# Kernel optimization log

Measured on AMD Instinct MI355X. Metric: run time of the kernel, lower is better.

The kernel has to match this reference:

```python
import jax, jax.numpy as jnp
import numpy as np
import math

B, S, D_MODEL = 8, 1024, 1024
N_INPUT, N_PROCESS = 256, 512
N_HEADS, N_HEADS_IN = 8, 4
HIDDEN = 2 * N_INPUT  # combination_analyzer hidden dim (default n_input*2)
TEMP = 2.0            # router temperature buffer


def _mha(x, w_in, b_in, w_out, b_out, n_heads):
    """torch nn.MultiheadAttention (batch_first, eval mode) self-attention."""
    Bq, Sq, E = x.shape
    qkv = x @ w_in.T + b_in                      # [B,S,3E]
    q, k, v = jnp.split(qkv, 3, axis=-1)
    dh = E // n_heads
    sh = lambda t: t.reshape(Bq, Sq, n_heads, dh).transpose(0, 2, 1, 3)
    q, k, v = sh(q), sh(k), sh(v)
    scores = jnp.einsum('bhqd,bhkd->bhqk', q, k) * (1.0 / math.sqrt(dh))
    attn = jax.nn.softmax(scores, axis=-1)
    out = jnp.einsum('bhqk,bhkd->bhqd', attn, v).transpose(0, 2, 1, 3).reshape(Bq, Sq, E)
    return out @ w_out.T + b_out


def _ln(x, g, b, eps=1e-5):
    m = x.mean(-1, keepdims=True)
    v = ((x - m) ** 2).mean(-1, keepdims=True)
    return (x - m) / jnp.sqrt(v + eps) * g + b


def setup_inputs() -> dict:
    key = jax.random.key(0)
    ks = jax.random.split(key, 24)
    rn = lambda i, shape, s=0.02: jax.random.normal(ks[i], shape, jnp.float32) * s
    return {
        'x': jax.random.normal(ks[0], (B, S, D_MODEL), jnp.float32),
        # DynamicRouter attention (embed=d_model, heads=8)
        'r_in_w': rn(1, (3 * D_MODEL, D_MODEL)), 'r_in_b': jnp.zeros((3 * D_MODEL,), jnp.float32),
        'r_out_w': rn(2, (D_MODEL, D_MODEL)), 'r_out_b': jnp.zeros((D_MODEL,), jnp.float32),
        'aff_w': rn(3, (N_INPUT, D_MODEL)), 'aff_b': jnp.zeros((N_INPUT,), jnp.float32),
        # InputNeurons
        'patterns': rn(4, (N_INPUT, D_MODEL), 0.05),
        'i_in_w': rn(5, (3 * N_INPUT, N_INPUT)), 'i_in_b': jnp.zeros((3 * N_INPUT,), jnp.float32),
        'i_out_w': rn(6, (N_INPUT, N_INPUT)), 'i_out_b': jnp.zeros((N_INPUT,), jnp.float32),
        'ln_g': jnp.ones((N_INPUT,), jnp.float32), 'ln_b': jnp.zeros((N_INPUT,), jnp.float32),
        # ProcessNeurons
        'comb_w': rn(7, (N_PROCESS, N_INPUT), 0.05),
        'out_proj_w': rn(8, (N_PROCESS, D_MODEL), 0.05),
        'a1_w': rn(9, (HIDDEN, N_INPUT)), 'a1_b': jnp.zeros((HIDDEN,), jnp.float32),
        'a2_w': rn(10, (N_PROCESS, HIDDEN)), 'a2_b': jnp.zeros((N_PROCESS,), jnp.float32),
        'k_input': 128, 'k_process': 256,
    }


def reference(x, r_in_w, r_in_b, r_out_w, r_out_b, aff_w, aff_b, patterns,
              i_in_w, i_in_b, i_out_w, i_out_b, ln_g, ln_b,
              comb_w, out_proj_w, a1_w, a1_b, a2_w, a2_b, k_input, k_process):
    Bq = x.shape[0]
    # ---- DynamicRouter (eval mode: no gumbel noise, no score noise) ----
    context = _mha(x, r_in_w, r_in_b, r_out_w, r_out_b, N_HEADS)      # [B,S,D]
    affinity = context @ aff_w.T + aff_b                              # [B,S,N_INPUT]
    scores = affinity.max(axis=1)                                     # [B,N_INPUT]
    logits = scores / TEMP
    soft_w = jax.nn.softmax(logits, axis=-1)
    _, indices = jax.lax.top_k(logits, k_input)                       # [B,k_in]
    mask = jnp.zeros_like(soft_w).at[jnp.arange(Bq)[:, None], indices].set(1.0)
    masked = soft_w * mask
    weights = masked / (masked.sum(-1, keepdims=True) + 1e-8)         # [B,N_INPUT]
    # ---- InputNeurons (eval: dropout off) ----
    acts = jax.nn.gelu(context @ patterns.T, approximate=False)       # [B,S,N_INPUT]
    attn_out = _mha(acts, i_in_w, i_in_b, i_out_w, i_out_b, N_HEADS_IN)
    acts = _ln(acts + attn_out, ln_g, ln_b)
    # ---- Gather routed input neurons, weighted by routing weights ----
    sel_acts = jnp.take_along_axis(acts, indices[:, None, :], axis=2)  # [B,S,k_in]
    sel_w = jnp.take_along_axis(weights, indices, axis=1)              # [B,k_in]
    sel_acts = sel_acts * sel_w[:, None, :]
    # ---- ProcessNeurons ----
    # selected_weights[b,p,j] = comb_w[p, indices[b,j]]
    sel_cw = jnp.take(comb_w, indices, axis=1).transpose(1, 0, 2)      # [B,P,k_in]
    proc_acts = jax.nn.gelu(jnp.einsum('bsk,bpk->bsp', sel_acts, sel_cw), approximate=False)
    input_sel = jnp.zeros((Bq, N_INPUT), jnp.float32).at[jnp.arange(Bq)[:, None], indices].set(1.0)
    relevance = jax.nn.gelu(input_sel @ a1_w.T + a1_b, approximate=False) @ a2_w.T + a2_b  # [B,P]
    act_scores = proc_acts.max(axis=1)                                 # [B,P]
    final_scores = act_scores * jax.nn.sigmoid(relevance)
    _, pidx = jax.lax.top_k(final_scores, k_process)                   # [B,k_p]
    sel_proc = jnp.take_along_axis(proc_acts, pidx[:, None, :], axis=2)  # [B,S,k_p]
    sel_proj = out_proj_w[pidx]                                        # [B,k_p,D]
    out = jnp.einsum('bsk,bkd->bsd', sel_proc, sel_proj)               # [B,S,D]
    # ---- residual (eval: dropout identity) ----
    return x + out
```

## Files before the change

### kernel.cpp

```cpp
#include <hip/hip_runtime.h>
#include <hip/hip_bf16.h>
#include <math.h>

constexpr int NB = 8, NS = 1024, ND = 1024, NIN = 256, NPROC = 512, KIN = 128, KPROC = 256;

typedef __attribute__((ext_vector_type(8))) short bf16x8;
typedef __attribute__((ext_vector_type(4))) float f32x4;

#define VMCNT(n) asm volatile("s_waitcnt vmcnt(" #n ")" ::: "memory")
#define LGKMCNT(n) asm volatile("s_waitcnt lgkmcnt(" #n ")" ::: "memory")

__device__ inline float gelu_f(float x) {
    return 0.5f * x * (1.0f + erff(x * 0.7071067811865476f));
}
__device__ inline unsigned short f2b(float f) {
    __hip_bfloat16 h = __float2bfloat16(f);
    return *reinterpret_cast<unsigned short*>(&h);
}
__device__ inline void gload16(const void* g, void* l) {
    __builtin_amdgcn_global_load_lds(
        (const __attribute__((address_space(1))) void*)g,
        (__attribute__((address_space(3))) void*)l, 16, 0, 0);
}

__global__ __launch_bounds__(256)
void cvt_all_kernel(const float* __restrict__ x, const float* __restrict__ rin,
                    const float* __restrict__ rout, const float* __restrict__ affw,
                    const float* __restrict__ patt, const float* __restrict__ iin,
                    const float* __restrict__ iout, const float* __restrict__ aff_b,
                    unsigned short* __restrict__ xb, unsigned short* __restrict__ rinb,
                    unsigned short* __restrict__ routb, unsigned short* __restrict__ affbw,
                    unsigned short* __restrict__ pattb, unsigned short* __restrict__ iinb,
                    unsigned short* __restrict__ ioutb, float* __restrict__ biascat)
{
    if (blockIdx.x == 0) {
        int t = threadIdx.x;
        biascat[t] = aff_b[t];
        biascat[256 + t] = 0.f;
    }
    long gi = (long)blockIdx.x * 256 + threadIdx.x;
    long stride = (long)gridDim.x * 256;
    for (; gi < 3342336; gi += stride) {
        const float4* s; ushort4* d; long off;
        if (gi < 2097152)      { s = (const float4*)x;    d = (ushort4*)xb;    off = gi; }
        else if (gi < 2883584) { s = (const float4*)rin;  d = (ushort4*)rinb;  off = gi - 2097152; }
        else if (gi < 3145728) { s = (const float4*)rout; d = (ushort4*)routb; off = gi - 2883584; }
        else if (gi < 3211264) { s = (const float4*)affw; d = (ushort4*)affbw; off = gi - 3145728; }
        else if (gi < 3276800) { s = (const float4*)patt; d = (ushort4*)pattb; off = gi - 3211264; }
        else if (gi < 3325952) { s = (const float4*)iin;  d = (ushort4*)iinb;  off = gi - 3276800; }
        else                   { s = (const float4*)iout; d = (ushort4*)ioutb; off = gi - 3325952; }
        float4 v = s[off];
        ushort4 o;
        o.x = f2b(v.x); o.y = f2b(v.y); o.z = f2b(v.z); o.w = f2b(v.w);
        d[off] = o;
    }
}

__global__ __launch_bounds__(256)
void gemm128s(const unsigned short* __restrict__ A, int lda,
              const unsigned short* __restrict__ B, int ldb,
              const float* __restrict__ bias,
              unsigned short* __restrict__ C16, int ldc,
              int K, int nbx)
{
    __shared__ __align__(16) unsigned short Ab[3][128 * 32];
    __shared__ __align__(16) unsigned short Bb[3][128 * 32];
    int o = blockIdx.x;
    int cpx = gridDim.x >> 3;
    int swz = (o & 7) * cpx + (o >> 3);
    int by = swz / nbx, bx = swz - by * nbx;
    int row0 = by * 128, col0 = bx * 128;

    int t = threadIdx.x;
    int w = t >> 6, l = t & 63, l15 = l & 15, g = l >> 4;
    int wr = w >> 1, wc = w & 1;
    int NT = K >> 5;

    f32x4 acc[4][4];
#pragma unroll
    for (int i = 0; i < 4; ++i)
#pragma unroll
        for (int j = 0; j < 4; ++j) acc[i][j] = (f32x4){0.f, 0.f, 0.f, 0.f};

    auto STAGE = [&](int c, int kt) {
        int k0 = kt * 32;
#pragma unroll
        for (int i = 0; i < 2; ++i) {
            int gi = t + i * 256;
            int row = gi >> 2, cg = gi & 3;
            int cgs = cg ^ ((row >> 1) & 3);
            gload16(&A[(long)(row0 + row) * lda + k0 + cgs * 8], &Ab[c][gi * 8]);
        }
#pragma unroll
        for (int i = 0; i < 2; ++i) {
            int gi = t + i * 256;
            int row = gi >> 2, cg = gi & 3;
            int cgs = cg ^ ((row >> 1) & 3);
            gload16(&B[(long)(col0 + row) * ldb + k0 + cgs * 8], &Bb[c][gi * 8]);
        }
    };

    STAGE(0, 0);
    STAGE(1, 1);

    int cbr = (g ^ ((l15 >> 1) & 3)) * 16;

    int cur = 0;
    for (int T = 0; T < NT; ++T) {
        if (T + 1 < NT) { VMCNT(4); } else { VMCNT(0); }
        __builtin_amdgcn_s_barrier();
        asm volatile("" ::: "memory");

        const char* Ab_ = (const char*)&Ab[cur][0];
        const char* Bb_ = (const char*)&Bb[cur][0];
        bf16x8 af[4], bfr[4];
#pragma unroll
        for (int mi = 0; mi < 4; ++mi)
            af[mi] = *(const bf16x8*)(Ab_ + (wr * 64 + mi * 16 + l15) * 64 + cbr);
#pragma unroll
        for (int ni = 0; ni < 4; ++ni)
            bfr[ni] = *(const bf16x8*)(Bb_ + (wc * 64 + ni * 16 + l15) * 64 + cbr);

        if (T + 2 < NT) {
            int nxt = cur + 2;
            if (nxt >= 3) nxt -= 3;
            STAGE(nxt, T + 2);
        }

        LGKMCNT(0);
        __builtin_amdgcn_sched_barrier(0);
        __builtin_amdgcn_s_setprio(1);
#pragma unroll
        for (int mi = 0; mi < 4; ++mi)
#pragma unroll
            for (int ni = 0; ni < 4; ++ni)
                acc[mi][ni] = __builtin_amdgcn_mfma_f32_16x16x32_bf16(
                    af[mi], bfr[ni], acc[mi][ni], 0, 0, 0);
        __builtin_amdgcn_s_setprio(0);

        cur = (cur == 2) ? 0 : cur + 1;
    }

#pragma unroll
    for (int mi = 0; mi < 4; ++mi) {
#pragma unroll
        for (int ni = 0; ni < 4; ++ni) {
            int col = col0 + wc * 64 + ni * 16 + l15;
            float bv = bias ? bias[col] : 0.f;
#pragma unroll
            for (int r = 0; r < 4; ++r) {
                int row = row0 + wr * 64 + mi * 16 + g * 4 + r;
                float v = acc[mi][ni][r] + bv;
                float vp = __shfl_xor(v, 1);
                if (!(l15 & 1)) {
                    unsigned int u = (unsigned int)f2b(v) | ((unsigned int)f2b(vp) << 16);
                    *(unsigned int*)&C16[(long)row * ldc + col] = u;
                }
            }
        }
    }
}

__global__ __launch_bounds__(256)
void gemm128x64(const unsigned short* __restrict__ A, int lda,
                const unsigned short* __restrict__ B, int ldb,
                const float* __restrict__ bias,
                unsigned short* __restrict__ C16, int ldc,
                int K, int nbx)
{
    __shared__ __align__(16) unsigned short Ab[3][128 * 32];
    __shared__ __align__(16) unsigned short Bb[3][64 * 32];
    int o = blockIdx.x;
    int cpx = gridDim.x >> 3;
    int swz = (o & 7) * cpx + (o >> 3);
    int by = swz / nbx, bx = swz - by * nbx;
    int row0 = by * 128, col0 = bx * 64;

    int t = threadIdx.x;
    int w = t >> 6, l = t & 63, l15 = l & 15, g = l >> 4;
    int wr = w >> 1, wc = w & 1;
    int NT = K >> 5;

    f32x4 acc[4][2];
#pragma unroll
    for (int i = 0; i < 4; ++i)
#pragma unroll
        for (int j = 0; j < 2; ++j) acc[i][j] = (f32x4){0.f, 0.f, 0.f, 0.f};

    auto STAGE = [&](int c, int kt) {
        int k0 = kt * 32;
#pragma unroll
        for (int i = 0; i < 2; ++i) {
            int gi = t + i * 256;
            int row = gi >> 2, cg = gi & 3;
            int cgs = cg ^ ((row >> 1) & 3);
            gload16(&A[(long)(row0 + row) * lda + k0 + cgs * 8], &Ab[c][gi * 8]);
        }
        {
            int gi = t;
            int row = gi >> 2, cg = gi & 3;
            int cgs = cg ^ ((row >> 1) & 3);
            gload16(&B[(long)(col0 + row) * ldb + k0 + cgs * 8], &Bb[c][gi * 8]);
        }
    };

    STAGE(0, 0);
    STAGE(1, 1);

    int cbr = (g ^ ((l15 >> 1) & 3)) * 16;

    int cur = 0;
    for (int T = 0; T < NT; ++T) {
        if (T + 1 < NT) { VMCNT(3); } else { VMCNT(0); }
        __builtin_amdgcn_s_barrier();
        asm volatile("" ::: "memory");

        const char* Ab_ = (const char*)&Ab[cur][0];
        const char* Bb_ = (const char*)&Bb[cur][0];
        bf16x8 af[4], bfr[2];
#pragma unroll
        for (int mi = 0; mi < 4; ++mi)
            af[mi] = *(const bf16x8*)(Ab_ + (wr * 64 + mi * 16 + l15) * 64 + cbr);
#pragma unroll
        for (int ni = 0; ni < 2; ++ni)
            bfr[ni] = *(const bf16x8*)(Bb_ + (wc * 32 + ni * 16 + l15) * 64 + cbr);

        if (T + 2 < NT) {
            int nxt = cur + 2;
            if (nxt >= 3) nxt -= 3;
            STAGE(nxt, T + 2);
        }

        LGKMCNT(0);
        __builtin_amdgcn_sched_barrier(0);
        __builtin_amdgcn_s_setprio(1);
#pragma unroll
        for (int mi = 0; mi < 4; ++mi)
#pragma unroll
            for (int ni = 0; ni < 2; ++ni)
                acc[mi][ni] = __builtin_amdgcn_mfma_f32_16x16x32_bf16(
                    af[mi], bfr[ni], acc[mi][ni], 0, 0, 0);
        __builtin_amdgcn_s_setprio(0);

        cur = (cur == 2) ? 0 : cur + 1;
    }

#pragma unroll
    for (int mi = 0; mi < 4; ++mi) {
#pragma unroll
        for (int ni = 0; ni < 2; ++ni) {
            int col = col0 + wc * 32 + ni * 16 + l15;
            float bv = bias ? bias[col] : 0.f;
#pragma unroll
            for (int r = 0; r < 4; ++r) {
                int row = row0 + wr * 64 + mi * 16 + g * 4 + r;
                float v = acc[mi][ni][r] + bv;
                float vp = __shfl_xor(v, 1);
                if (!(l15 & 1)) {
                    unsigned int u = (unsigned int)f2b(v) | ((unsigned int)f2b(vp) << 16);
                    *(unsigned int*)&C16[(long)row * ldc + col] = u;
                }
            }
        }
    }
}

__global__ __launch_bounds__(256)
void gemm_bf16(const unsigned short* __restrict__ A, long sA, int lda,
               const unsigned short* __restrict__ B, long sB, int ldb,
               const float* __restrict__ bias,
               const float* __restrict__ resid, long sR, int ldr,
               float* __restrict__ C32, long sC32, int ldc32,
               unsigned short* __restrict__ C16, long sC16, int ldc16,
               float* __restrict__ C32b, int ldc32b,
               int M, int N, int K, int act)
{
    __shared__ __align__(16) unsigned short As[128 * 64];
    __shared__ __align__(16) unsigned short Bs[128 * 64];
    int bz = blockIdx.z;
    const unsigned short* Abp = A + (long)bz * sA;
    const unsigned short* Bbp = B + (long)bz * sB;
    int row0 = blockIdx.y * 128, col0 = blockIdx.x * 128;
    int t = threadIdx.x;
    int w = t >> 6, l = t & 63, l15 = l & 15, g = l >> 4;
    int wr = w >> 1, wc = w & 1;
    int srow = l >> 3;
    int scol = (l & 7) * 8;
    f32x4 zero4 = {0.f, 0.f, 0.f, 0.f};
    f32x4 acc[4][4];
#pragma unroll
    for (int i = 0; i < 4; ++i)
#pragma unroll
        for (int j = 0; j < 4; ++j) acc[i][j] = zero4;

    for (int k0 = 0; k0 < K; k0 += 64) {
        __syncthreads();
#pragma unroll
        for (int c = 0; c < 4; ++c) {
            int r = w * 32 + c * 8;
            gload16(&Abp[(long)(row0 + r + srow) * lda + k0 + scol], &As[r * 64]);
            gload16(&Bbp[(long)(col0 + r + srow) * ldb + k0 + scol], &Bs[r * 64]);
        }
        __syncthreads();
        bf16x8 af[4][2], bfr[4][2];
#pragma unroll
        for (int mi = 0; mi < 4; ++mi)
#pragma unroll
            for (int ks = 0; ks < 2; ++ks) {
                af[mi][ks] = *(const bf16x8*)&As[(wr * 64 + mi * 16 + l15) * 64 + g * 8 + ks * 32];
                bfr[mi][ks] = *(const bf16x8*)&Bs[(wc * 64 + mi * 16 + l15) * 64 + g * 8 + ks * 32];
            }
#pragma unroll
        for (int ks = 0; ks < 2; ++ks)
#pragma unroll
            for (int mi = 0; mi < 4; ++mi)
#pragma unroll
                for (int ni = 0; ni < 4; ++ni)
                    acc[mi][ni] = __builtin_amdgcn_mfma_f32_16x16x32_bf16(af[mi][ks], bfr[ni][ks], acc[mi][ni], 0, 0, 0);
    }

#pragma unroll
    for (int mi = 0; mi < 4; ++mi) {
#pragma unroll
        for (int ni = 0; ni < 4; ++ni) {
#pragma unroll
            for (int r = 0; r < 4; ++r) {
                int row = row0 + wr * 64 + mi * 16 + g * 4 + r;
                int col = col0 + wc * 64 + ni * 16 + l15;
                float v = acc[mi][ni][r];
                if (bias) v += bias[col];
                if (act == 2) {
                    if (col < 256) {
                        C32[(long)row * ldc32 + col] = v;
                    } else {
                        v = gelu_f(v);
                        C32b[(long)row * ldc32b + (col - 256)] = v;
                        C16[(long)row * ldc16 + (col - 256)] = f2b(v);
                    }
                    continue;
                }
                if (act == 1) v = gelu_f(v);
                if (resid) v += resid[(long)bz * sR + (long)row * ldr + col];
                if (C32) C32[(long)bz * sC32 + (long)row * ldc32 + col] = v;
                if (C16) C16[(long)bz * sC16 + (long)row * ldc16 + col] = f2b(v);
            }
        }
    }
}

template <int D>
__global__ __launch_bounds__(256, 2)
void attn_mfma(unsigned short* __restrict__ qkv, int stride, int koff, int voff, float scale)
{
    constexpr int GRL = D / 8;
    constexpr int NITK = (64 * GRL) / 256;
    constexpr int NITV = NITK;
    constexpr int NKS = D / 32;
    constexpr int NF = D / 16;
    constexpr int LV = 72;
    constexpr int LP = 72;
    constexpr int NT = NS / 64;

    __shared__ __align__(16) unsigned short Ks[2][64 * D];
    __shared__ __align__(16) unsigned short Vt[D * LV];
    __shared__ __align__(16) unsigned short Ps[128 * LP];

    int b = blockIdx.z, h = blockIdx.y, qt = blockIdx.x;
    int t = threadIdx.x, w = t >> 6, l = t & 63, l15 = l & 15, g = l >> 4;
    int wq = w * 32;
    long qbase = ((long)b * NS + qt * 128) * stride + h * D;
    long kvbase = (long)b * NS * stride + h * D;

    bf16x8 qreg[2][NKS];
#pragma unroll
    for (int qh = 0; qh < 2; ++qh)
#pragma unroll
        for (int ks = 0; ks < NKS; ++ks)
            qreg[qh][ks] = *(const bf16x8*)&qkv[qbase + (long)(wq + qh * 16 + l15) * stride + g * 8 + ks * 32];

    auto KSTAGE = [&](int c, int kt) {
#pragma unroll
        for (int i = 0; i < NITK; ++i) {
            int gi = t + i * 256;
            int row = gi / GRL, cg = gi % GRL;
            int cgs = cg ^ (row & 7);
            gload16(&qkv[kvbase + (long)(kt * 64 + row) * stride + koff + cgs * 8],
                    &Ks[c][gi * 8]);
        }
    };
    uint4 vp[NITV];
    auto VLOAD = [&](int kt) {
#pragma unroll
        for (int i = 0; i < NITV; ++i) {
            int vgi = t + i * 256;
            int kc = vgi & 63, db = vgi >> 6;
            vp[i] = *(const uint4*)&qkv[kvbase + (long)(kt * 64 + kc) * stride + voff + db * 8];
        }
    };
    auto VWRITE = [&]() {
#pragma unroll
        for (int i = 0; i < NITV; ++i) {
            int vgi = t + i * 256;
            int kc = vgi & 63, db = vgi >> 6;
            uint4 v = vp[i];
            Vt[(db * 8 + 0) * LV + kc] = (unsigned short)(v.x & 0xffff);
            Vt[(db * 8 + 1) * LV + kc] = (unsigned short)(v.x >> 16);
            Vt[(db * 8 + 2) * LV + kc] = (unsigned short)(v.y & 0xffff);
            Vt[(db * 8 + 3) * LV + kc] = (unsigned short)(v.y >> 16);
            Vt[(db * 8 + 4) * LV + kc] = (unsigned short)(v.z & 0xffff);
            Vt[(db * 8 + 5) * LV + kc] = (unsigned short)(v.z >> 16);
            Vt[(db * 8 + 6) * LV + kc] = (unsigned short)(v.w & 0xffff);
            Vt[(db * 8 + 7) * LV + kc] = (unsigned short)(v.w >> 16);
        }
    };

    KSTAGE(0, 0);
    VLOAD(0);
    KSTAGE(1, 1);
    if constexpr (NITK == 4) { VMCNT(4); } else { VMCNT(2); }
    VWRITE();
    LGKMCNT(0);
    __builtin_amdgcn_sched_barrier(0);
    __builtin_amdgcn_s_barrier();

    float m_run[2] = {-INFINITY, -INFINITY};
    float l_run[2] = {0.f, 0.f};
    f32x4 zero4 = {0.f, 0.f, 0.f, 0.f};
    f32x4 oacc[2][NF];
#pragma unroll
    for (int qh = 0; qh < 2; ++qh)
#pragma unroll
        for (int nf = 0; nf < NF; ++nf) oacc[qh][nf] = zero4;

    int xr = (l15 & 7) << 4;
    for (int kt = 0; kt < NT; ++kt) {
        if (kt + 1 < NT) VLOAD(kt + 1);

        const char* ksb = (const char*)&Ks[kt & 1][0];
        f32x4 st[4][2];
#pragma unroll
        for (int f = 0; f < 4; ++f)
#pragma unroll
            for (int qh = 0; qh < 2; ++qh) st[f][qh] = zero4;
#pragma unroll
        for (int ks = 0; ks < NKS; ++ks) {
#pragma unroll
            for (int f = 0; f < 4; ++f) {
                int cb = (g * 16 + ks * 64) ^ xr;
                bf16x8 a = *(const bf16x8*)(ksb + (f * 16 + l15) * (D * 2) + cb);
#pragma unroll
                for (int qh = 0; qh < 2; ++qh)
                    st[f][qh] = __builtin_amdgcn_mfma_f32_16x16x32_bf16(a, qreg[qh][ks], st[f][qh], 0, 0, 0);
            }
        }
#pragma unroll
        for (int qh = 0; qh < 2; ++qh) {
            float pm = -INFINITY;
#pragma unroll
            for (int f = 0; f < 4; ++f) {
                st[f][qh] *= scale;
#pragma unroll
                for (int r = 0; r < 4; ++r) pm = fmaxf(pm, st[f][qh][r]);
            }
            pm = fmaxf(pm, __shfl_xor(pm, 16));
            pm = fmaxf(pm, __shfl_xor(pm, 32));
            float mn = fmaxf(m_run[qh], pm);
            float corr = __expf(m_run[qh] - mn);
            float rs = 0.f;
#pragma unroll
            for (int f = 0; f < 4; ++f) {
                float p0 = __expf(st[f][qh][0] - mn);
                float p1 = __expf(st[f][qh][1] - mn);
                float p2 = __expf(st[f][qh][2] - mn);
                float p3 = __expf(st[f][qh][3] - mn);
                rs += (p0 + p1) + (p2 + p3);
                ushort4 pw;
                pw.x = f2b(p0); pw.y = f2b(p1); pw.z = f2b(p2); pw.w = f2b(p3);
                *(ushort4*)&Ps[(wq + qh * 16 + l15) * LP + f * 16 + g * 4] = pw;
            }
            rs += __shfl_xor(rs, 16);
            rs += __shfl_xor(rs, 32);
            l_run[qh] = l_run[qh] * corr + rs;
            m_run[qh] = mn;
            float corrO[4];
#pragma unroll
            for (int r = 0; r < 4; ++r) corrO[r] = __shfl(corr, g * 4 + r);
#pragma unroll
            for (int nf = 0; nf < NF; ++nf)
#pragma unroll
                for (int r = 0; r < 4; ++r) oacc[qh][nf][r] *= corrO[r];
        }
#pragma unroll
        for (int ks2 = 0; ks2 < 2; ++ks2) {
            bf16x8 vb[NF];
#pragma unroll
            for (int nf = 0; nf < NF; ++nf)
                vb[nf] = *(const bf16x8*)&Vt[(nf * 16 + l15) * LV + ks2 * 32 + g * 8];
#pragma unroll
            for (int qh = 0; qh < 2; ++qh) {
                bf16x8 pa = *(const bf16x8*)&Ps[(wq + qh * 16 + l15) * LP + ks2 * 32 + g * 8];
#pragma unroll
                for (int nf = 0; nf < NF; ++nf)
                    oacc[qh][nf] = __builtin_amdgcn_mfma_f32_16x16x32_bf16(pa, vb[nf], oacc[qh][nf], 0, 0, 0);
            }
        }

        if (kt + 1 < NT) {
            LGKMCNT(0);
            __builtin_amdgcn_sched_barrier(0);
            __builtin_amdgcn_s_barrier();
            if (kt + 2 < NT) {
                KSTAGE(kt & 1, kt + 2);
                if constexpr (NITK == 4) { VMCNT(4); } else { VMCNT(2); }
            } else {
                VMCNT(0);
            }
            VWRITE();
            LGKMCNT(0);
            __builtin_amdgcn_sched_barrier(0);
            __builtin_amdgcn_s_barrier();
        }
    }

#pragma unroll
    for (int qh = 0; qh < 2; ++qh) {
        float lo[4];
#pragma unroll
        for (int r = 0; r < 4; ++r) lo[r] = __shfl(l_run[qh], g * 4 + r);
#pragma unroll
        for (int nf = 0; nf < NF; ++nf)
#pragma unroll
            for (int r = 0; r < 4; ++r) {
                float o = oacc[qh][nf][r] / lo[r];
                qkv[qbase + (long)(wq + qh * 16 + g * 4 + r) * stride + nf * 16 + l15] = f2b(o);
            }
    }
}

__global__ __launch_bounds__(256)
void maxpart_aff_kernel(const float* __restrict__ aff, float* __restrict__ part)
{
    int sc = blockIdx.x, b = blockIdx.y, t = threadIdx.x;
    float m = -INFINITY;
    for (int s = sc * 32; s < (sc + 1) * 32; ++s)
        m = fmaxf(m, aff[((long)b * NS + s) * NIN + t]);
    part[(b * 32 + sc) * NIN + t] = m;
}

__global__ __launch_bounds__(256)
void rank_input_kernel(const float* __restrict__ part, int* __restrict__ idx_out,
                       float* __restrict__ w_out)
{
    int b = blockIdx.x, t = threadIdx.x;
    __shared__ float lg[256], rv[256];
    float m = part[(b * 32) * NIN + t];
#pragma unroll
    for (int sc = 1; sc < 32; ++sc) m = fmaxf(m, part[(b * 32 + sc) * NIN + t]);
    float l = m * 0.5f;
    lg[t] = l;
    rv[t] = l;
    __syncthreads();
    for (int off = 128; off; off >>= 1) {
        if (t < off) rv[t] = fmaxf(rv[t], rv[t + off]);
        __syncthreads();
    }
    float mx = rv[0];
    __syncthreads();
    float e = expf(l - mx);
    rv[t] = e;
    __syncthreads();
    for (int off = 128; off; off >>= 1) {
        if (t < off) rv[t] += rv[t + off];
        __syncthreads();
    }
    float Zs = rv[0];
    float soft = e / Zs;
    __syncthreads();
    int rank = 0;
    for (int j = 0; j < 256; ++j) {
        float vj = lg[j];
        rank += (vj > l) || (vj == l && j < t);
    }
    rv[t] = (rank < KIN) ? soft : 0.f;
    __syncthreads();
    for (int off = 128; off; off >>= 1) {
        if (t < off) rv[t] += rv[t + off];
        __syncthreads();
    }
    float msum = rv[0];
    if (rank < KIN) {
        idx_out[b * KIN + rank] = t;
        w_out[b * KIN + rank] = soft / (msum + 1e-8f);
    }
}

__global__ __launch_bounds__(512)
void rank_proc_kernel(const float* __restrict__ finals, int* __restrict__ pidx)
{
    int b = blockIdx.x, t = threadIdx.x;
    __shared__ float v[512];
    float xv = finals[b * NPROC + t];
    v[t] = xv;
    __syncthreads();
    int rank = 0;
    for (int j = 0; j < 512; ++j) {
        float vj = v[j];
        rank += (vj > xv) || (vj == xv && j < t);
    }
    if (rank < KPROC) pidx[b * KPROC + rank] = t;
}

__global__ __launch_bounds__(256)
void ln_gather_kernel(const float* __restrict__ a, const float* __restrict__ bsrc,
                      const float* __restrict__ gg, const float* __restrict__ be,
                      const int* __restrict__ idx_in, const float* __restrict__ w_sel,
                      unsigned short* __restrict__ sel_acts)
{
    long row = blockIdx.x;
    int b = blockIdx.x >> 10;
    int t = threadIdx.x;
    float v = a[row * 256 + t] + bsrc[row * 256 + t];
    __shared__ float rv[256];
    __shared__ float lnv[256];
    rv[t] = v;
    __syncthreads();
    for (int off = 128; off; off >>= 1) {
        if (t < off) rv[t] += rv[t + off];
        __syncthreads();
    }
    float mean = rv[0] * (1.f / 256.f);
    __syncthreads();
    float d = v - mean;
    rv[t] = d * d;
    __syncthreads();
    for (int off = 128; off; off >>= 1) {
        if (t < off) rv[t] += rv[t + off];
        __syncthreads();
    }
    float var = rv[0] * (1.f / 256.f);
    lnv[t] = d * rsqrtf(var + 1e-5f) * gg[t] + be[t];
    __syncthreads();
    if (t < KIN) {
        int id = idx_in[b * KIN + t];
        sel_acts[row * KIN + t] = f2b(lnv[id] * w_sel[b * KIN + t]);
    }
}

__global__ void gather_sel_cw_b(const float* __restrict__ comb_w, const int* __restrict__ idx_in,
                                unsigned short* __restrict__ sel_cw)
{
    int gidx = blockIdx.x * 256 + threadIdx.x;
    int b = gidx >> 16;
    int rem = gidx & 65535;
    int pb = rem >> 7, j = rem & 127;
    sel_cw[gidx] = f2b(comb_w[pb * NIN + idx_in[b * KIN + j]]);
}

__global__ void gather_sel_proc_b(const float* __restrict__ proc_acts, const int* __restrict__ pidx,
                                  unsigned short* __restrict__ sel_proc)
{
    int s = blockIdx.x, b = blockIdx.y, j = threadIdx.x;
    long row = (long)b * NS + s;
    sel_proc[row * KPROC + j] = f2b(proc_acts[row * NPROC + pidx[b * KPROC + j]]);
}

__global__ void gather_sel_projT(const float* __restrict__ out_proj_w, const int* __restrict__ pidx,
                                 unsigned short* __restrict__ selT)
{
    int gidx = blockIdx.x * 256 + threadIdx.x;
    int b = gidx >> 15;
    int rem = gidx & 32767;
    int d = rem >> 5;
    int kp0 = (rem & 31) * 8;
    unsigned int u[4];
#pragma unroll
    for (int i = 0; i < 4; ++i) {
        unsigned short e0 = f2b(out_proj_w[(long)pidx[b * KPROC + kp0 + 2 * i] * ND + d]);
        unsigned short e1 = f2b(out_proj_w[(long)pidx[b * KPROC + kp0 + 2 * i + 1] * ND + d]);
        u[i] = (unsigned int)e0 | ((unsigned int)e1 << 16);
    }
    uint4 o; o.x = u[0]; o.y = u[1]; o.z = u[2]; o.w = u[3];
    *(uint4*)&selT[((long)b * ND + d) * KPROC + kp0] = o;
}

__global__ __launch_bounds__(512)
void maxpart_kernel(const float* __restrict__ proc, float* __restrict__ part)
{
    int sc = blockIdx.x, b = blockIdx.y, t = threadIdx.x;
    float m = -INFINITY;
    for (int s = sc * 32; s < (sc + 1) * 32; ++s)
        m = fmaxf(m, proc[((long)b * NS + s) * NPROC + t]);
    part[(b * 32 + sc) * NPROC + t] = m;
}

__global__ __launch_bounds__(512)
void relevance_kernel(const float* __restrict__ part, const int* __restrict__ idx_in,
                      const float* __restrict__ a1w, const float* __restrict__ a1b,
                      const float* __restrict__ a2w, const float* __restrict__ a2b,
                      float* __restrict__ finals)
{
    int b = blockIdx.x, t = threadIdx.x;
    float m = part[(b * 32) * NPROC + t];
#pragma unroll
    for (int sc = 1; sc < 32; ++sc) m = fmaxf(m, part[(b * 32 + sc) * NPROC + t]);
    __shared__ float rel1[512];
    __shared__ int sidx[KIN];
    if (t < KIN) sidx[t] = idx_in[b * KIN + t];
    __syncthreads();
    float r1 = a1b[t];
    const float* a1row = a1w + (long)t * NIN;
    for (int j = 0; j < KIN; ++j) r1 += a1row[sidx[j]];
    rel1[t] = gelu_f(r1);
    __syncthreads();
    float r = a2b[t];
    const float* a2row = a2w + (long)t * 512;
    for (int hh = 0; hh < 512; ++hh) r += rel1[hh] * a2row[hh];
    float sig = 1.f / (1.f + expf(-r));
    finals[b * NPROC + t] = m * sig;
}

extern "C" void kernel_launch(void* const* d_in, const int* in_sizes, int n_in,
                              void* d_out, int out_size, void* d_ws, size_t ws_size,
                              hipStream_t stream)
{
    const float* x       = (const float*)d_in[0];
    const float* r_in_w  = (const float*)d_in[1];
    const float* r_in_b  = (const float*)d_in[2];
    const float* r_out_w = (const float*)d_in[3];
    const float* r_out_b = (const float*)d_in[4];
    const float* aff_w   = (const float*)d_in[5];
    const float* aff_b   = (const float*)d_in[6];
    const float* patterns= (const float*)d_in[7];
    const float* i_in_w  = (const float*)d_in[8];
    const float* i_in_b  = (const float*)d_in[9];
    const float* i_out_w = (const float*)d_in[10];
    const float* i_out_b = (const float*)d_in[11];
    const float* ln_g    = (const float*)d_in[12];
    const float* ln_b    = (const float*)d_in[13];
    const float* comb_w  = (const float*)d_in[14];
    const float* out_proj_w = (const float*)d_in[15];
    const float* a1w     = (const float*)d_in[16];
    const float* a1b     = (const float*)d_in[17];
    const float* a2w     = (const float*)d_in[18];
    const float* a2b     = (const float*)d_in[19];
    float* out = (float*)d_out;

    char* ws = (char*)d_ws;
    unsigned short* qkv1b    = (unsigned short*)(ws + 0);
    unsigned short* contextb = (unsigned short*)(ws + 50331648);
    unsigned short* xb       = (unsigned short*)(ws + 67108864);
    unsigned short* w_rin_b  = (unsigned short*)(ws + 83886080);
    unsigned short* w_rout_b = (unsigned short*)(ws + 90177536);
    unsigned short* w_aff_b  = (unsigned short*)(ws + 92274688);
    unsigned short* patt_b   = (unsigned short*)(ws + 92798976);
    unsigned short* w_iin_b  = (unsigned short*)(ws + 93323264);
    unsigned short* w_iout_b = (unsigned short*)(ws + 93716480);
    float* w_sel   = (float*)(ws + 93855744);
    int*   idx_in  = (int*)(ws + 93859840);
    float* finals  = (float*)(ws + 93863936);
    int*   pidx    = (int*)(ws + 93880320);
    float* affin   = (float*)(ws + 94019584);
    float* acts0   = (float*)(ws + 102408192);
    unsigned short* acts0b = (unsigned short*)(ws + 110796800);
    unsigned short* qkv2b  = (unsigned short*)(ws + 114991104);
    float* attn2proj = (float*)(ws + 0);
    float* proc_acts = (float*)(ws + 16777216);
    unsigned short* sel_actsb = (unsigned short*)(ws + 33554432);
    unsigned short* sel_cwb   = (unsigned short*)(ws + 35651584);
    unsigned short* sel_procb = (unsigned short*)(ws + 36700160);
    unsigned short* sel_projT = (unsigned short*)(ws + 40894464);
    float* biascat  = (float*)(ws + 45088768);
    float* part_aff = (float*)(ws + 45091840);
    float* maxpart  = (float*)(ws + 45353984);

    cvt_all_kernel<<<2048, 256, 0, stream>>>(
        x, r_in_w, r_out_w, aff_w, patterns, i_in_w, i_out_w, aff_b,
        xb, w_rin_b, w_rout_b, w_aff_b, patt_b, w_iin_b, w_iout_b, biascat);

    gemm128s<<<1536, 256, 0, stream>>>(xb, ND, w_rin_b, ND, r_in_b, qkv1b, 3 * ND, ND, 24);
    attn_mfma<128><<<dim3(8, 8, 8), 256, 0, stream>>>(qkv1b, 3 * ND, ND, 2 * ND, 0.088388347648318447f);
    gemm128x64<<<1024, 256, 0, stream>>>(qkv1b, 3 * ND, w_rout_b, ND, r_out_b, contextb, ND, ND, 16);
    gemm_bf16<<<dim3(4, 64, 1), 256, 0, stream>>>(
        contextb, 0, ND, w_aff_b, 0, ND, biascat, nullptr, 0, 0,
        affin, 0, NIN, acts0b, 0, NIN, acts0, NIN, NB * NS, 2 * NIN, ND, 2);
    maxpart_aff_kernel<<<dim3(32, NB), 256, 0, stream>>>(affin, part_aff);
    rank_input_kernel<<<NB, 256, 0, stream>>>(part_aff, idx_in, w_sel);
    gemm128x64<<<768, 256, 0, stream>>>(acts0b, NIN, w_iin_b, NIN, i_in_b, qkv2b, 3 * NIN, NIN, 12);
    attn_mfma<64><<<dim3(8, 4, 8), 256, 0, stream>>>(qkv2b, 3 * NIN, NIN, 2 * NIN, 0.125f);
    gemm_bf16<<<dim3(2, 64, 1), 256, 0, stream>>>(
        qkv2b, 0, 3 * NIN, w_iout_b, 0, NIN, i_out_b, nullptr, 0, 0,
        attn2proj, 0, NIN, nullptr, 0, 0, nullptr, 0, NB * NS, NIN, NIN, 0);
    ln_gather_kernel<<<NB * NS, 256, 0, stream>>>(acts0, attn2proj, ln_g, ln_b,
                                                  idx_in, w_sel, sel_actsb);
    gather_sel_cw_b<<<2048, 256, 0, stream>>>(comb_w, idx_in, sel_cwb);
    gemm_bf16<<<dim3(4, 8, NB), 256, 0, stream>>>(
        sel_actsb, (long)NS * KIN, KIN, sel_cwb, (long)NPROC * KIN, KIN,
        nullptr, nullptr, 0, 0,
        proc_acts, (long)NS * NPROC, NPROC, nullptr, 0, 0, nullptr, 0, NS, NPROC, KIN, 1);
    maxpart_kernel<<<dim3(32, NB), 512, 0, stream>>>(proc_acts, maxpart);
    relevance_kernel<<<NB, 512, 0, stream>>>(maxpart, idx_in, a1w, a1b, a2w, a2b, finals);
    rank_proc_kernel<<<NB, 512, 0, stream>>>(finals, pidx);
    gather_sel_proc_b<<<dim3(NS, NB), KPROC, 0, stream>>>(proc_acts, pidx, sel_procb);
    gather_sel_projT<<<1024, 256, 0, stream>>>(out_proj_w, pidx, sel_projT);
    gemm_bf16<<<dim3(8, 8, NB), 256, 0, stream>>>(
        sel_procb, (long)NS * KPROC, KPROC, sel_projT, (long)ND * KPROC, KPROC,
        nullptr, x, (long)NS * ND, ND,
        out, (long)NS * ND, ND, nullptr, 0, 0, nullptr, 0, NS, ND, KPROC, 0);
    (void)in_sizes; (void)n_in; (void)out_size; (void)ws_size;
}
```

Before: 487.7 us.

## Replace generic bf16 GEMM with triple-buffered 128x64 tiled kernel with swizzled LDS

```diff
diff --git a/kernel.cpp b/kernel.cpp
--- a/kernel.cpp
+++ b/kernel.cpp
@@ -266,69 +266,105 @@
 }
 
 __global__ __launch_bounds__(256)
-void gemm_bf16(const unsigned short* __restrict__ A, long sA, int lda,
-               const unsigned short* __restrict__ B, long sB, int ldb,
-               const float* __restrict__ bias,
-               const float* __restrict__ resid, long sR, int ldr,
-               float* __restrict__ C32, long sC32, int ldc32,
-               unsigned short* __restrict__ C16, long sC16, int ldc16,
-               float* __restrict__ C32b, int ldc32b,
-               int M, int N, int K, int act)
-{
-    __shared__ __align__(16) unsigned short As[128 * 64];
-    __shared__ __align__(16) unsigned short Bs[128 * 64];
+void gemm128e(const unsigned short* __restrict__ A, long sA, int lda,
+              const unsigned short* __restrict__ B, long sB, int ldb,
+              const float* __restrict__ bias,
+              const float* __restrict__ resid, long sR, int ldr,
+              float* __restrict__ C32, long sC32, int ldc32,
+              unsigned short* __restrict__ C16, long sC16, int ldc16,
+              float* __restrict__ C32b, int ldc32b,
+              int K, int nbx, int act)
+{
+    __shared__ __align__(16) unsigned short Ab[3][128 * 32];
+    __shared__ __align__(16) unsigned short Bb[3][64 * 32];
     int bz = blockIdx.z;
-    const unsigned short* Abp = A + (long)bz * sA;
-    const unsigned short* Bbp = B + (long)bz * sB;
-    int row0 = blockIdx.y * 128, col0 = blockIdx.x * 128;
+    const unsigned short* Abase = A + (long)bz * sA;
+    const unsigned short* Bbase = B + (long)bz * sB;
+    int o = blockIdx.x;
+    int cpx = gridDim.x >> 3;
+    int swz = (o & 7) * cpx + (o >> 3);
+    int by = swz / nbx, bx = swz - by * nbx;
+    int row0 = by * 128, col0 = bx * 64;
+
     int t = threadIdx.x;
     int w = t >> 6, l = t & 63, l15 = l & 15, g = l >> 4;
     int wr = w >> 1, wc = w & 1;
-    int srow = l >> 3;
-    int scol = (l & 7) * 8;
-    f32x4 zero4 = {0.f, 0.f, 0.f, 0.f};
-    f32x4 acc[4][4];
+    int NT = K >> 5;
+
+    f32x4 acc[4][2];
 #pragma unroll
     for (int i = 0; i < 4; ++i)
 #pragma unroll
-        for (int j = 0; j < 4; ++j) acc[i][j] = zero4;
-
-    for (int k0 = 0; k0 < K; k0 += 64) {
-        __syncthreads();
-#pragma unroll
-        for (int c = 0; c < 4; ++c) {
-            int r = w * 32 + c * 8;
-            gload16(&Abp[(long)(row0 + r + srow) * lda + k0 + scol], &As[r * 64]);
-            gload16(&Bbp[(long)(col0 + r + srow) * ldb + k0 + scol], &Bs[r * 64]);
-        }
-        __syncthreads();
-        bf16x8 af[4][2], bfr[4][2];
+        for (int j = 0; j < 2; ++j) acc[i][j] = (f32x4){0.f, 0.f, 0.f, 0.f};
+
+    auto STAGE = [&](int c, int kt) {
+        int k0 = kt * 32;
+#pragma unroll
+        for (int i = 0; i < 2; ++i) {
+            int gi = t + i * 256;
+            int row = gi >> 2, cg = gi & 3;
+            int cgs = cg ^ ((row >> 1) & 3);
+            gload16(&Abase[(long)(row0 + row) * lda + k0 + cgs * 8], &Ab[c][gi * 8]);
+        }
+        {
+            int gi = t;
+            int row = gi >> 2, cg = gi & 3;
+            int cgs = cg ^ ((row >> 1) & 3);
+            gload16(&Bbase[(long)(col0 + row) * ldb + k0 + cgs * 8], &Bb[c][gi * 8]);
+        }
+    };
+
+    STAGE(0, 0);
+    STAGE(1, 1);
+
+    int cbr = (g ^ ((l15 >> 1) & 3)) * 16;
+
+    int cur = 0;
+    for (int T = 0; T < NT; ++T) {
+        if (T + 1 < NT) { VMCNT(3); } else { VMCNT(0); }
+        __builtin_amdgcn_s_barrier();
+        asm volatile("" ::: "memory");
+
+        const char* Ab_ = (const char*)&Ab[cur][0];
+        const char* Bb_ = (const char*)&Bb[cur][0];
+        bf16x8 af[4], bfr[2];
 #pragma unroll
         for (int mi = 0; mi < 4; ++mi)
-#pragma unroll
-            for (int ks = 0; ks < 2; ++ks) {
-                af[mi][ks] = *(const bf16x8*)&As[(wr * 64 + mi * 16 + l15) * 64 + g * 8 + ks * 32];
-                bfr[mi][ks] = *(const bf16x8*)&Bs[(wc * 64 + mi * 16 + l15) * 64 + g * 8 + ks * 32];
-            }
-#pragma unroll
-        for (int ks = 0; ks < 2; ++ks)
-#pragma unroll
-            for (int mi = 0; mi < 4; ++mi)
-#pragma unroll
-                for (int ni = 0; ni < 4; ++ni)
-                    acc[mi][ni] = __builtin_amdgcn_mfma_f32_16x16x32_bf16(af[mi][ks], bfr[ni][ks], acc[mi][ni], 0, 0, 0);
+            af[mi] = *(const bf16x8*)(Ab_ + (wr * 64 + mi * 16 + l15) * 64 + cbr);
+#pragma unroll
+        for (int ni = 0; ni < 2; ++ni)
+            bfr[ni] = *(const bf16x8*)(Bb_ + (wc * 32 + ni * 16 + l15) * 64 + cbr);
+
+        if (T + 2 < NT) {
+            int nxt = cur + 2;
+            if (nxt >= 3) nxt -= 3;
+            STAGE(nxt, T + 2);
+        }
+
+        LGKMCNT(0);
+        __builtin_amdgcn_sched_barrier(0);
+        __builtin_amdgcn_s_setprio(1);
+#pragma unroll
+        for (int mi = 0; mi < 4; ++mi)
+#pragma unroll
+            for (int ni = 0; ni < 2; ++ni)
+                acc[mi][ni] = __builtin_amdgcn_mfma_f32_16x16x32_bf16(
+                    af[mi], bfr[ni], acc[mi][ni], 0, 0, 0);
+        __builtin_amdgcn_s_setprio(0);
+
+        cur = (cur == 2) ? 0 : cur + 1;
     }
 
 #pragma unroll
     for (int mi = 0; mi < 4; ++mi) {
 #pragma unroll
-        for (int ni = 0; ni < 4; ++ni) {
+        for (int ni = 0; ni < 2; ++ni) {
+            int col = col0 + wc * 32 + ni * 16 + l15;
+            float bv = bias ? bias[col] : 0.f;
 #pragma unroll
             for (int r = 0; r < 4; ++r) {
                 int row = row0 + wr * 64 + mi * 16 + g * 4 + r;
-                int col = col0 + wc * 64 + ni * 16 + l15;
-                float v = acc[mi][ni][r];
-                if (bias) v += bias[col];
+                float v = acc[mi][ni][r] + bv;
                 if (act == 2) {
                     if (col < 256) {
                         C32[(long)row * ldc32 + col] = v;
@@ -780,31 +816,31 @@
     gemm128s<<<1536, 256, 0, stream>>>(xb, ND, w_rin_b, ND, r_in_b, qkv1b, 3 * ND, ND, 24);
     attn_mfma<128><<<dim3(8, 8, 8), 256, 0, stream>>>(qkv1b, 3 * ND, ND, 2 * ND, 0.088388347648318447f);
     gemm128x64<<<1024, 256, 0, stream>>>(qkv1b, 3 * ND, w_rout_b, ND, r_out_b, contextb, ND, ND, 16);
-    gemm_bf16<<<dim3(4, 64, 1), 256, 0, stream>>>(
+    gemm128e<<<dim3(512, 1, 1), 256, 0, stream>>>(
         contextb, 0, ND, w_aff_b, 0, ND, biascat, nullptr, 0, 0,
-        affin, 0, NIN, acts0b, 0, NIN, acts0, NIN, NB * NS, 2 * NIN, ND, 2);
+        affin, 0, NIN, acts0b, 0, NIN, acts0, NIN, ND, 8, 2);
     maxpart_aff_kernel<<<dim3(32, NB), 256, 0, stream>>>(affin, part_aff);
     rank_input_kernel<<<NB, 256, 0, stream>>>(part_aff, idx_in, w_sel);
     gemm128x64<<<768, 256, 0, stream>>>(acts0b, NIN, w_iin_b, NIN, i_in_b, qkv2b, 3 * NIN, NIN, 12);
     attn_mfma<64><<<dim3(8, 4, 8), 256, 0, stream>>>(qkv2b, 3 * NIN, NIN, 2 * NIN, 0.125f);
-    gemm_bf16<<<dim3(2, 64, 1), 256, 0, stream>>>(
+    gemm128e<<<dim3(256, 1, 1), 256, 0, stream>>>(
         qkv2b, 0, 3 * NIN, w_iout_b, 0, NIN, i_out_b, nullptr, 0, 0,
-        attn2proj, 0, NIN, nullptr, 0, 0, nullptr, 0, NB * NS, NIN, NIN, 0);
+        attn2proj, 0, NIN, nullptr, 0, 0, nullptr, 0, NIN, 4, 0);
     ln_gather_kernel<<<NB * NS, 256, 0, stream>>>(acts0, attn2proj, ln_g, ln_b,
                                                   idx_in, w_sel, sel_actsb);
     gather_sel_cw_b<<<2048, 256, 0, stream>>>(comb_w, idx_in, sel_cwb);
-    gemm_bf16<<<dim3(4, 8, NB), 256, 0, stream>>>(
+    gemm128e<<<dim3(64, 1, NB), 256, 0, stream>>>(
         sel_actsb, (long)NS * KIN, KIN, sel_cwb, (long)NPROC * KIN, KIN,
         nullptr, nullptr, 0, 0,
-        proc_acts, (long)NS * NPROC, NPROC, nullptr, 0, 0, nullptr, 0, NS, NPROC, KIN, 1);
+        proc_acts, (long)NS * NPROC, NPROC, nullptr, 0, 0, nullptr, 0, KIN, 8, 1);
     maxpart_kernel<<<dim3(32, NB), 512, 0, stream>>>(proc_acts, maxpart);
     relevance_kernel<<<NB, 512, 0, stream>>>(maxpart, idx_in, a1w, a1b, a2w, a2b, finals);
     rank_proc_kernel<<<NB, 512, 0, stream>>>(finals, pidx);
     gather_sel_proc_b<<<dim3(NS, NB), KPROC, 0, stream>>>(proc_acts, pidx, sel_procb);
     gather_sel_projT<<<1024, 256, 0, stream>>>(out_proj_w, pidx, sel_projT);
-    gemm_bf16<<<dim3(8, 8, NB), 256, 0, stream>>>(
+    gemm128e<<<dim3(128, 1, NB), 256, 0, stream>>>(
         sel_procb, (long)NS * KPROC, KPROC, sel_projT, (long)ND * KPROC, KPROC,
         nullptr, x, (long)NS * ND, ND,
-        out, (long)NS * ND, ND, nullptr, 0, 0, nullptr, 0, NS, ND, KPROC, 0);
+        out, (long)NS * ND, ND, nullptr, 0, 0, nullptr, 0, KPROC, 16, 0);
     (void)in_sizes; (void)n_in; (void)out_size; (void)ws_size;
 }
```

Measured after the change: 427.8 us. 1.14x faster.
